# Kernel tuning notes

Measured on AMD Instinct MI355X. Metric: run time of the kernel, lower is better.

Reference implementation:

```python
import jax, jax.numpy as jnp
import numpy as np

N_HEAD, D_MODEL, D_K, D_V, D_O = 16, 1024, 64, 64, 1024
B, S = 4, 2048


def setup_inputs() -> dict:
    key = jax.random.key(0)
    ks = jax.random.split(key, 11)
    s = 0.02
    return {
        "q": jax.random.normal(ks[0], (B, S, D_MODEL), jnp.float32),
        "k": jax.random.normal(ks[1], (B, S, D_MODEL), jnp.float32),
        "v": jax.random.normal(ks[2], (B, S, D_MODEL), jnp.float32),
        "Wq": jax.random.normal(ks[3], (D_MODEL, N_HEAD * D_K), jnp.float32) * s,
        "bq": jnp.zeros((N_HEAD * D_K,), jnp.float32),
        "Wk": jax.random.normal(ks[4], (D_MODEL, N_HEAD * D_K), jnp.float32) * s,
        "bk": jnp.zeros((N_HEAD * D_K,), jnp.float32),
        "Wv": jax.random.normal(ks[5], (D_MODEL, N_HEAD * D_V), jnp.float32) * s,
        "bv": jnp.zeros((N_HEAD * D_V,), jnp.float32),
        "Wo": jax.random.normal(ks[6], (N_HEAD * D_V, D_O), jnp.float32) * s,
        "bo": jnp.zeros((D_O,), jnp.float32),
    }


def reference(q, k, v, Wq, bq, Wk, bk, Wv, bv, Wo, bo):
    b, n_q, _ = q.shape
    # QKV projections -> [b, s, h, d]
    qh = (q @ Wq + bq).reshape(b, -1, N_HEAD, D_K)
    kh = (k @ Wk + bk).reshape(b, -1, N_HEAD, D_K)
    vh = (v @ Wv + bv).reshape(b, -1, N_HEAD, D_V)
    scale = jnp.asarray(np.power(D_K, 0.5), qh.dtype)
    # scores [b, h, n_q, n_k]
    scores = jnp.einsum("bqhd,bkhd->bhqk", qh, kh) / scale
    attn = jax.nn.softmax(scores, axis=-1)
    out = jnp.einsum("bhqk,bkhd->bqhd", attn, vh).reshape(b, n_q, N_HEAD * D_V)
    return out @ Wo + bo
```

## Files before the change

kernel.cpp:

```cpp
#include <hip/hip_runtime.h>
#include <hip/hip_bf16.h>


typedef __attribute__((ext_vector_type(8))) short bf16x8;
typedef __attribute__((ext_vector_type(4))) float f32x4;
typedef __attribute__((ext_vector_type(4))) unsigned short u16x4;

#define QSCALE 0.1803368801111244f

__device__ __forceinline__ unsigned short f2bf(float x) {
  __hip_bfloat16 h = __float2bfloat16(x);
  return __builtin_bit_cast(unsigned short, h);
}

__device__ __forceinline__ short f2bf_s(float x) {
  return (short)f2bf(x);
}

__device__ __forceinline__ float fexp2(float x) {
#if __has_builtin(__builtin_amdgcn_exp2f)
  return __builtin_amdgcn_exp2f(x);
#else
  return exp2f(x);
#endif
}

__global__ void wtrans4(const float* __restrict__ W0, const float* __restrict__ W1,
                        const float* __restrict__ W2, const float* __restrict__ W3,
                        unsigned short* __restrict__ WT) {
  __shared__ float t[32][33];
  int x = threadIdx.x, y = threadIdx.y;
  int k0 = blockIdx.x * 32, n0 = blockIdx.y * 32;
  int z = blockIdx.z;
  const float* W = z == 0 ? W0 : z == 1 ? W1 : z == 2 ? W2 : W3;
  float scale = z == 0 ? QSCALE : 1.0f;
  unsigned short* dst = WT + (size_t)z * (1024 * 1024);
#pragma unroll
  for (int i = 0; i < 4; i++)
    t[y + i * 8][x] = W[(k0 + y + i * 8) * 1024 + n0 + x];
  __syncthreads();
#pragma unroll
  for (int i = 0; i < 4; i++)
    dst[(n0 + y + i * 8) * 1024 + k0 + x] = f2bf(t[x][y + i * 8] * scale);
}

template <bool AF32, int MODE>
__global__ __launch_bounds__(256, 2) void gemm128(
    const void* __restrict__ Ap, const unsigned short* __restrict__ BT,
    const float* __restrict__ bias, float bscale, void* __restrict__ Cp) {
  __shared__ __align__(16) char As[8192];
  __shared__ __align__(16) char Bs[8192];
  const int K = 1024;
  int tid = threadIdx.x;
  int lane = tid & 63;
  int w = tid >> 6;
  int wr = w >> 1, wc = w & 1;
  int bid = blockIdx.x;
  int sid = (bid & 7) * 64 + (bid >> 3);
  int m0 = (sid >> 3) * 128, n0 = (sid & 7) * 128;
  int r = tid >> 1;
  int kb = (tid & 1) << 4;

  f32x4 acc[4][4];
#pragma unroll
  for (int i = 0; i < 4; i++)
#pragma unroll
    for (int j = 0; j < 4; j++) acc[i][j] = (f32x4){0.f, 0.f, 0.f, 0.f};

  const float* Af = (const float*)Ap;
  const unsigned short* Ab = (const unsigned short*)Ap;

  f32x4 afr[4];
  bf16x8 afb[2];
  bf16x8 bfr[2];

  if (AF32) {
    const f32x4* p = (const f32x4*)(Af + (size_t)(m0 + r) * K + kb);
#pragma unroll
    for (int i = 0; i < 4; i++) afr[i] = p[i];
  } else {
    const bf16x8* p = (const bf16x8*)(Ab + (size_t)(m0 + r) * K + kb);
    afb[0] = p[0]; afb[1] = p[1];
  }
  {
    const bf16x8* p = (const bf16x8*)(BT + (size_t)(n0 + r) * K + kb);
    bfr[0] = p[0]; bfr[1] = p[1];
  }

  int swz = (r & 7) << 4;
  int wbyte = r * 64 + kb * 2;
  int cc = lane & 15, g = lane >> 4;

  for (int k0 = 0; k0 < K; k0 += 32) {
    __syncthreads();
    if (AF32) {
      bf16x8 s0, s1;
#pragma unroll
      for (int i = 0; i < 8; i++) {
        s0[i] = f2bf_s(afr[i >> 2][i & 3]);
        s1[i] = f2bf_s(afr[2 + (i >> 2)][i & 3]);
      }
      *(bf16x8*)(As + (wbyte ^ swz)) = s0;
      *(bf16x8*)(As + ((wbyte + 16) ^ swz)) = s1;
    } else {
      *(bf16x8*)(As + (wbyte ^ swz)) = afb[0];
      *(bf16x8*)(As + ((wbyte + 16) ^ swz)) = afb[1];
    }
    *(bf16x8*)(Bs + (wbyte ^ swz)) = bfr[0];
    *(bf16x8*)(Bs + ((wbyte + 16) ^ swz)) = bfr[1];
    if (k0 + 32 < K) {
      if (AF32) {
        const f32x4* p = (const f32x4*)(Af + (size_t)(m0 + r) * K + k0 + 32 + kb);
#pragma unroll
        for (int i = 0; i < 4; i++) afr[i] = p[i];
      } else {
        const bf16x8* p = (const bf16x8*)(Ab + (size_t)(m0 + r) * K + k0 + 32 + kb);
        afb[0] = p[0]; afb[1] = p[1];
      }
      const bf16x8* p = (const bf16x8*)(BT + (size_t)(n0 + r) * K + k0 + 32 + kb);
      bfr[0] = p[0]; bfr[1] = p[1];
    }
    __syncthreads();
    bf16x8 a[4], b[4];
#pragma unroll
    for (int mi = 0; mi < 4; mi++) {
      int row = wr * 64 + mi * 16 + cc;
      int byte = (row * 64 + g * 16) ^ ((row & 7) << 4);
      a[mi] = *(const bf16x8*)(As + byte);
    }
#pragma unroll
    for (int ni = 0; ni < 4; ni++) {
      int row = wc * 64 + ni * 16 + cc;
      int byte = (row * 64 + g * 16) ^ ((row & 7) << 4);
      b[ni] = *(const bf16x8*)(Bs + byte);
    }
#pragma unroll
    for (int mi = 0; mi < 4; mi++)
#pragma unroll
      for (int ni = 0; ni < 4; ni++)
        acc[mi][ni] =
            __builtin_amdgcn_mfma_f32_16x16x32_bf16(a[mi], b[ni], acc[mi][ni], 0, 0, 0);
  }

#pragma unroll
  for (int ni = 0; ni < 4; ni++) {
    int n = n0 + wc * 64 + ni * 16 + cc;
    float bv = bias[n] * bscale;
#pragma unroll
    for (int mi = 0; mi < 4; mi++) {
      int mbase = m0 + wr * 64 + mi * 16 + g * 4;
      if (MODE == 2) {
        u16x4 pk;
#pragma unroll
        for (int j = 0; j < 4; j++) pk[j] = f2bf(acc[mi][ni][j] + bv);
        int bb = mbase >> 11, s = mbase & 2047;
        int sp = (s & ~31) | ((((s & 15) >> 2) << 3) + (((s >> 4) & 1) << 2));
        int hh = n >> 6, d = n & 63;
        *(u16x4*)&((unsigned short*)Cp)[(((size_t)(bb * 16 + hh) * 64 + d) << 11) + sp] = pk;
      } else {
#pragma unroll
        for (int j = 0; j < 4; j++) {
          float val = acc[mi][ni][j] + bv;
          int m = mbase + j;
          if (MODE == 0) {
            int bb = m >> 11, s = m & 2047;
            int hh = n >> 6, d = n & 63;
            ((unsigned short*)Cp)[(((bb * 16 + hh) * 2048 + s) << 6) + d] = f2bf(val);
          } else {
            ((float*)Cp)[(size_t)m * 1024 + n] = val;
          }
        }
      }
    }
  }
}

__global__ __launch_bounds__(256, 4) void attn64(
    const unsigned short* __restrict__ Qh, const unsigned short* __restrict__ Kh,
    const unsigned short* __restrict__ Vt, unsigned short* __restrict__ O) {
  __shared__ __align__(16) char Ks[2][8192];
  __shared__ __align__(16) char Vs[2][8192];
  int tid = threadIdx.x, lane = tid & 63, w = tid >> 6;
  int bid = blockIdx.x;
  int sid = (bid & 7) * 128 + (bid >> 3);
  int bh = sid >> 4, qb = sid & 15;
  int b = bh >> 4, h = bh & 15;
  const unsigned short* Q  = Qh + (size_t)bh * (2048 * 64);
  const unsigned short* Kb = Kh + (size_t)bh * (2048 * 64);
  const unsigned short* Vb = Vt + (size_t)bh * (64 * 2048);
  int q0 = qb * 128 + w * 32;
  int cc = lane & 15, g = lane >> 4, g4 = g << 2;

  bf16x8 vones;
#pragma unroll
  for (int i = 0; i < 8; i++) vones[i] = (short)0x3F80;

  bf16x8 aq0[2], aq1[2];
#pragma unroll
  for (int g2 = 0; g2 < 2; g2++) {
    aq0[g2] = *(const bf16x8*)(Q + (size_t)(q0 + cc) * 64 + g2 * 32 + g * 8);
    aq1[g2] = *(const bf16x8*)(Q + (size_t)(q0 + 16 + cc) * 64 + g2 * 32 + g * 8);
  }

  f32x4 oacc0[4], oacc1[4];
#pragma unroll
  for (int df = 0; df < 4; df++) {
    oacc0[df] = (f32x4){0.f, 0.f, 0.f, 0.f};
    oacc1[df] = (f32x4){0.f, 0.f, 0.f, 0.f};
  }
  f32x4 lacc0 = (f32x4){0.f, 0.f, 0.f, 0.f};
  f32x4 lacc1 = (f32x4){0.f, 0.f, 0.f, 0.f};

  int kr = tid >> 2, kq = tid & 3;
  int kswz = (kr & 7) << 4;
  int kbyte = kr * 128 + kq * 32;

  bf16x8 kv[2], vv[2];
  {
    const bf16x8* pK = (const bf16x8*)(Kb + (size_t)kr * 64 + kq * 16);
    const bf16x8* pV = (const bf16x8*)(Vb + (size_t)kr * 2048 + kq * 16);
    kv[0] = pK[0]; kv[1] = pK[1];
    vv[0] = pV[0]; vv[1] = pV[1];
  }
#pragma unroll
  for (int i = 0; i < 2; i++) {
    *(bf16x8*)(Ks[0] + ((kbyte + i * 16) ^ kswz)) = kv[i];
    *(bf16x8*)(Vs[0] + ((kbyte + i * 16) ^ kswz)) = vv[i];
  }
  int cur = 0;

  for (int kt = 0; kt < 2048; kt += 64) {
    __syncthreads();
    if (kt + 64 < 2048) {
      const bf16x8* pK = (const bf16x8*)(Kb + (size_t)(kt + 64 + kr) * 64 + kq * 16);
      const bf16x8* pV = (const bf16x8*)(Vb + (size_t)kr * 2048 + kt + 64 + kq * 16);
      kv[0] = pK[0]; kv[1] = pK[1];
      vv[0] = pV[0]; vv[1] = pV[1];
    }
    const char* Kc = Ks[cur];
    const char* Vc = Vs[cur];

    f32x4 sc0[4], sc1[4];
#pragma unroll
    for (int nf = 0; nf < 4; nf++) {
      sc0[nf] = (f32x4){0.f, 0.f, 0.f, 0.f};
      sc1[nf] = (f32x4){0.f, 0.f, 0.f, 0.f};
    }
    __builtin_amdgcn_s_setprio(1);
#pragma unroll
    for (int nf = 0; nf < 4; nf++) {
#pragma unroll
      for (int g2 = 0; g2 < 2; g2++) {
        int rk = nf * 16 + cc;
        int byte = (rk * 128 + g2 * 64 + g * 16) ^ ((rk & 7) << 4);
        bf16x8 bk = *(const bf16x8*)(Kc + byte);
        sc0[nf] = __builtin_amdgcn_mfma_f32_16x16x32_bf16(bk, aq0[g2], sc0[nf], 0, 0, 0);
        sc1[nf] = __builtin_amdgcn_mfma_f32_16x16x32_bf16(bk, aq1[g2], sc1[nf], 0, 0, 0);
      }
    }
    __builtin_amdgcn_s_setprio(0);

#pragma unroll
    for (int nf = 0; nf < 4; nf++)
#pragma unroll
      for (int t = 0; t < 4; t++) {
        sc0[nf][t] = fexp2(sc0[nf][t]);
        sc1[nf][t] = fexp2(sc1[nf][t]);
      }

    bf16x8 pa0[2], pa1[2];
#pragma unroll
    for (int kk = 0; kk < 2; kk++) {
#pragma unroll
      for (int i = 0; i < 4; i++) {
        pa0[kk][i]     = f2bf_s(sc0[2 * kk][i]);
        pa0[kk][4 + i] = f2bf_s(sc0[2 * kk + 1][i]);
        pa1[kk][i]     = f2bf_s(sc1[2 * kk][i]);
        pa1[kk][4 + i] = f2bf_s(sc1[2 * kk + 1][i]);
      }
    }
    __builtin_amdgcn_s_setprio(1);
#pragma unroll
    for (int df = 0; df < 4; df++) {
#pragma unroll
      for (int kk = 0; kk < 2; kk++) {
        int rv = df * 16 + cc;
        int byte = (rv * 128 + kk * 64 + g * 16) ^ ((rv & 7) << 4);
        bf16x8 bv = *(const bf16x8*)(Vc + byte);
        oacc0[df] = __builtin_amdgcn_mfma_f32_16x16x32_bf16(pa0[kk], bv, oacc0[df], 0, 0, 0);
        oacc1[df] = __builtin_amdgcn_mfma_f32_16x16x32_bf16(pa1[kk], bv, oacc1[df], 0, 0, 0);
      }
    }
#pragma unroll
    for (int kk = 0; kk < 2; kk++) {
      lacc0 = __builtin_amdgcn_mfma_f32_16x16x32_bf16(pa0[kk], vones, lacc0, 0, 0, 0);
      lacc1 = __builtin_amdgcn_mfma_f32_16x16x32_bf16(pa1[kk], vones, lacc1, 0, 0, 0);
    }
    __builtin_amdgcn_s_setprio(0);

    if (kt + 64 < 2048) {
      char* Kn = Ks[cur ^ 1];
      char* Vn = Vs[cur ^ 1];
#pragma unroll
      for (int i = 0; i < 2; i++) {
        *(bf16x8*)(Kn + ((kbyte + i * 16) ^ kswz)) = kv[i];
        *(bf16x8*)(Vn + ((kbyte + i * 16) ^ kswz)) = vv[i];
      }
    }
    cur ^= 1;
  }

#pragma unroll
  for (int t = 0; t < 4; t++) {
    float inv0 = 1.0f / lacc0[t];
    float inv1 = 1.0f / lacc1[t];
    int srow = q0 + g4 + t;
#pragma unroll
    for (int df = 0; df < 4; df++) {
      int d = df * 16 + cc;
      O[((size_t)b * 2048 + srow) * 1024 + h * 64 + d]      = f2bf(oacc0[df][t] * inv0);
      O[((size_t)b * 2048 + srow + 16) * 1024 + h * 64 + d] = f2bf(oacc1[df][t] * inv1);
    }
  }
}

extern "C" void kernel_launch(void* const* d_in, const int* in_sizes, int n_in,
                              void* d_out, int out_size, void* d_ws, size_t ws_size,
                              hipStream_t stream) {
  const float* q  = (const float*)d_in[0];
  const float* k  = (const float*)d_in[1];
  const float* v  = (const float*)d_in[2];
  const float* Wq = (const float*)d_in[3];
  const float* bq = (const float*)d_in[4];
  const float* Wk = (const float*)d_in[5];
  const float* bk = (const float*)d_in[6];
  const float* Wv = (const float*)d_in[7];
  const float* bv = (const float*)d_in[8];
  const float* Wo = (const float*)d_in[9];
  const float* bo = (const float*)d_in[10];

  char* ws = (char*)d_ws;
  const size_t MB = 1024 * 1024;
  unsigned short* WqT = (unsigned short*)(ws + 0 * MB);
  unsigned short* WkT = (unsigned short*)(ws + 2 * MB);
  unsigned short* WvT = (unsigned short*)(ws + 4 * MB);
  unsigned short* WoT = (unsigned short*)(ws + 6 * MB);
  unsigned short* qh  = (unsigned short*)(ws + 8 * MB);
  unsigned short* kh  = (unsigned short*)(ws + 24 * MB);
  unsigned short* vt  = (unsigned short*)(ws + 40 * MB);
  unsigned short* ao  = (unsigned short*)(ws + 56 * MB);

  wtrans4<<<dim3(32, 32, 4), dim3(32, 8), 0, stream>>>(Wq, Wk, Wv, Wo, WqT);

  gemm128<true, 0><<<512, 256, 0, stream>>>(q, WqT, bq, QSCALE, qh);
  gemm128<true, 0><<<512, 256, 0, stream>>>(k, WkT, bk, 1.0f, kh);
  gemm128<true, 2><<<512, 256, 0, stream>>>(v, WvT, bv, 1.0f, vt);

  attn64<<<1024, 256, 0, stream>>>(qh, kh, vt, ao);

  gemm128<false, 1><<<512, 256, 0, stream>>>(ao, WoT, bo, 1.0f, d_out);
}
```

Before: 200.6 us.

## Double-buffer LDS tiles in gemm128 to drop one barrier per k-step

Splits the A and B shared-memory tiles into two ping-pong buffers. The next tile is written to the alternate buffer after the MFMAs, which leaves one __syncthreads per iteration instead of two and lets the global-load latency overlap with compute. LDS offsets are also precomputed outside the loop. LDS use doubles to 32KB per block, which could limit occupancy at 2 blocks per CU.

```diff
diff --git a/kernel.cpp b/kernel.cpp
--- a/kernel.cpp
+++ b/kernel.cpp
@@ -48,8 +48,8 @@
 __global__ __launch_bounds__(256, 2) void gemm128(
     const void* __restrict__ Ap, const unsigned short* __restrict__ BT,
     const float* __restrict__ bias, float bscale, void* __restrict__ Cp) {
-  __shared__ __align__(16) char As[8192];
-  __shared__ __align__(16) char Bs[8192];
+  __shared__ __align__(16) char As[2][8192];
+  __shared__ __align__(16) char Bs[2][8192];
   const int K = 1024;
   int tid = threadIdx.x;
   int lane = tid & 63;
@@ -91,23 +91,37 @@
   int wbyte = r * 64 + kb * 2;
   int cc = lane & 15, g = lane >> 4;
 
+  int abyte[4], bbyte[4];
+#pragma unroll
+  for (int mi = 0; mi < 4; mi++) {
+    int row = wr * 64 + mi * 16 + cc;
+    abyte[mi] = (row * 64 + g * 16) ^ ((row & 7) << 4);
+  }
+#pragma unroll
+  for (int ni = 0; ni < 4; ni++) {
+    int row = wc * 64 + ni * 16 + cc;
+    bbyte[ni] = (row * 64 + g * 16) ^ ((row & 7) << 4);
+  }
+
+  if (AF32) {
+    bf16x8 s0, s1;
+#pragma unroll
+    for (int i = 0; i < 8; i++) {
+      s0[i] = f2bf_s(afr[i >> 2][i & 3]);
+      s1[i] = f2bf_s(afr[2 + (i >> 2)][i & 3]);
+    }
+    *(bf16x8*)(As[0] + (wbyte ^ swz)) = s0;
+    *(bf16x8*)(As[0] + ((wbyte + 16) ^ swz)) = s1;
+  } else {
+    *(bf16x8*)(As[0] + (wbyte ^ swz)) = afb[0];
+    *(bf16x8*)(As[0] + ((wbyte + 16) ^ swz)) = afb[1];
+  }
+  *(bf16x8*)(Bs[0] + (wbyte ^ swz)) = bfr[0];
+  *(bf16x8*)(Bs[0] + ((wbyte + 16) ^ swz)) = bfr[1];
+  int cur = 0;
+
   for (int k0 = 0; k0 < K; k0 += 32) {
     __syncthreads();
-    if (AF32) {
-      bf16x8 s0, s1;
-#pragma unroll
-      for (int i = 0; i < 8; i++) {
-        s0[i] = f2bf_s(afr[i >> 2][i & 3]);
-        s1[i] = f2bf_s(afr[2 + (i >> 2)][i & 3]);
-      }
-      *(bf16x8*)(As + (wbyte ^ swz)) = s0;
-      *(bf16x8*)(As + ((wbyte + 16) ^ swz)) = s1;
-    } else {
-      *(bf16x8*)(As + (wbyte ^ swz)) = afb[0];
-      *(bf16x8*)(As + ((wbyte + 16) ^ swz)) = afb[1];
-    }
-    *(bf16x8*)(Bs + (wbyte ^ swz)) = bfr[0];
-    *(bf16x8*)(Bs + ((wbyte + 16) ^ swz)) = bfr[1];
     if (k0 + 32 < K) {
       if (AF32) {
         const f32x4* p = (const f32x4*)(Af + (size_t)(m0 + r) * K + k0 + 32 + kb);
@@ -120,26 +134,41 @@
       const bf16x8* p = (const bf16x8*)(BT + (size_t)(n0 + r) * K + k0 + 32 + kb);
       bfr[0] = p[0]; bfr[1] = p[1];
     }
-    __syncthreads();
+    const char* Ac = As[cur];
+    const char* Bc = Bs[cur];
+
     bf16x8 a[4], b[4];
 #pragma unroll
-    for (int mi = 0; mi < 4; mi++) {
-      int row = wr * 64 + mi * 16 + cc;
-      int byte = (row * 64 + g * 16) ^ ((row & 7) << 4);
-      a[mi] = *(const bf16x8*)(As + byte);
-    }
-#pragma unroll
-    for (int ni = 0; ni < 4; ni++) {
-      int row = wc * 64 + ni * 16 + cc;
-      int byte = (row * 64 + g * 16) ^ ((row & 7) << 4);
-      b[ni] = *(const bf16x8*)(Bs + byte);
-    }
+    for (int mi = 0; mi < 4; mi++) a[mi] = *(const bf16x8*)(Ac + abyte[mi]);
+#pragma unroll
+    for (int ni = 0; ni < 4; ni++) b[ni] = *(const bf16x8*)(Bc + bbyte[ni]);
 #pragma unroll
     for (int mi = 0; mi < 4; mi++)
 #pragma unroll
       for (int ni = 0; ni < 4; ni++)
         acc[mi][ni] =
             __builtin_amdgcn_mfma_f32_16x16x32_bf16(a[mi], b[ni], acc[mi][ni], 0, 0, 0);
+
+    if (k0 + 32 < K) {
+      char* An = As[cur ^ 1];
+      char* Bn = Bs[cur ^ 1];
+      if (AF32) {
+        bf16x8 s0, s1;
+#pragma unroll
+        for (int i = 0; i < 8; i++) {
+          s0[i] = f2bf_s(afr[i >> 2][i & 3]);
+          s1[i] = f2bf_s(afr[2 + (i >> 2)][i & 3]);
+        }
+        *(bf16x8*)(An + (wbyte ^ swz)) = s0;
+        *(bf16x8*)(An + ((wbyte + 16) ^ swz)) = s1;
+      } else {
+        *(bf16x8*)(An + (wbyte ^ swz)) = afb[0];
+        *(bf16x8*)(An + ((wbyte + 16) ^ swz)) = afb[1];
+      }
+      *(bf16x8*)(Bn + (wbyte ^ swz)) = bfr[0];
+      *(bf16x8*)(Bn + ((wbyte + 16) ^ swz)) = bfr[1];
+    }
+    cur ^= 1;
   }
 
 #pragma unroll
```

Result: slower. 206.0 us (+2.7%).
